# Kernel tuning notes

Hardware: AMD Instinct MI355X
Metric: run time of the kernel (lower is better)

Reference implementation:

```python
import jax, jax.numpy as jnp
import numpy as np

B, D = 1024, 768


def setup_inputs() -> dict:
    key = jax.random.key(0)
    k1, k2 = jax.random.split(key)
    image_features = jax.random.normal(k1, (B, D), dtype=jnp.float32)
    # plant a few exact duplicate rows so the label-propagation path is nontrivial
    image_features = image_features.at[17].set(image_features[3])
    image_features = image_features.at[512].set(image_features[3])
    image_features = image_features.at[900].set(image_features[128])
    text_features = jax.random.normal(k2, (B, D), dtype=jnp.float32)
    logit_scale = jnp.float32(14.285714)  # exp(log(1/0.07)), standard CLIP init
    return {"image_features": image_features, "text_features": text_features, "logit_scale": logit_scale}


def reference(image_features, text_features, logit_scale):
    # logits_per_image: [B, B]
    logits = logit_scale * (image_features @ text_features.T)
    # Duplicate detection: the original O(B^2) python loop assigns to row j the
    # index of the FIRST row i (i <= j) whose features exactly equal row j.
    # eq[i, j] = rows i and j are elementwise identical
    eq = jnp.all(image_features[:, None, :] == image_features[None, :, :], axis=-1)  # [B, B] bool
    labels = jnp.argmax(eq, axis=0)  # first matching index per row (diag guarantees a hit)
    # cross-entropy with integer labels, mean over batch
    logp = jax.nn.log_softmax(logits, axis=1)
    loss = -jnp.mean(jnp.take_along_axis(logp, labels[:, None], axis=1))
    return loss
```

## Files before the change

kernel.cpp:

```cpp
#include <hip/hip_runtime.h>
#include <stdint.h>

#define BATCH 1024
#define DIM 768

typedef unsigned long long u64;
typedef __attribute__((ext_vector_type(8))) short short8;
typedef __attribute__((ext_vector_type(4))) float f32x4;

#define WS_ACC  8192
#define WS_PMAX 12288
#define WS_PSUM 28672
#define WS_TXTB 49152

__device__ __forceinline__ unsigned short to_bf16(float x) {
    unsigned int u = __float_as_uint(x);
    return (unsigned short)((u + 0x7FFFu + ((u >> 16) & 1u)) >> 16);
}

__global__ __launch_bounds__(256) void prep_kernel(
        const float* __restrict__ img, const float* __restrict__ txt,
        u64* __restrict__ hashes, float* __restrict__ acc, int* __restrict__ counter,
        unsigned short* __restrict__ txtB) {
    if (blockIdx.x == 0 && threadIdx.x == 0) { *acc = 0.0f; *counter = 0; }
    const int wave = threadIdx.x >> 6;
    const int lane = threadIdx.x & 63;

    for (int i = wave; i < 6; i += 4) {
        const int G  = blockIdx.x * 6 + i;
        const int tt = G / 24;
        const int g  = G - tt * 24;
        const int col = tt * 16 + (lane & 15);
        const int k0  = g * 32 + (lane >> 4) * 8;
        const float4 va = *(const float4*)(txt + (size_t)col * DIM + k0);
        const float4 vb = *(const float4*)(txt + (size_t)col * DIM + k0 + 4);
        short8 hv = {(short)to_bf16(va.x), (short)to_bf16(va.y),
                     (short)to_bf16(va.z), (short)to_bf16(va.w),
                     (short)to_bf16(vb.x), (short)to_bf16(vb.y),
                     (short)to_bf16(vb.z), (short)to_bf16(vb.w)};
        *(short8*)(txtB + (size_t)(g * 64 + tt) * 512 + lane * 8) = hv;
    }

    const int row = blockIdx.x * 4 + wave;
    const float4* rp = (const float4*)(img + (size_t)row * DIM);
    u64 h = 0;
#pragma unroll
    for (int c = 0; c < 3; ++c) {
        float4 v = rp[c * 64 + lane];
        int p = c * 256 + lane * 4;
        h += ((u64)__float_as_uint(v.x) + 0x9E3779B97F4A7C15ULL) * (u64)(2 * p + 1);
        h += ((u64)__float_as_uint(v.y) + 0x9E3779B97F4A7C15ULL) * (u64)(2 * p + 3);
        h += ((u64)__float_as_uint(v.z) + 0x9E3779B97F4A7C15ULL) * (u64)(2 * p + 5);
        h += ((u64)__float_as_uint(v.w) + 0x9E3779B97F4A7C15ULL) * (u64)(2 * p + 7);
    }
#pragma unroll
    for (int m = 32; m; m >>= 1) h += __shfl_xor(h, m, 64);
    if (lane == 0) hashes[row] = h;
}

__global__ __launch_bounds__(1024) void gemm_kernel(
        const float* __restrict__ img, const float* __restrict__ scale_p,
        const unsigned short* __restrict__ txtB,
        float* __restrict__ pmax, float* __restrict__ psum) {
    __shared__ unsigned short Ahi[16 * DIM];
    __shared__ float logitsS[16 * 260];

    const int tid  = threadIdx.x;
    const int wave = tid >> 6;
    const int lane = tid & 63;
    const int quad = lane >> 4;
    const int l15  = lane & 15;
    const int r0    = (blockIdx.x >> 2) * 16;
    const int chunk = blockIdx.x & 3;

    {
        const float* ir = img + (size_t)(r0 + wave) * DIM;
#pragma unroll
        for (int j = 0; j < 12; ++j) {
            const int k = lane + j * 64;
            Ahi[((k >> 3) * 16 + wave) * 8 + (k & 7)] = to_bf16(ir[k]);
        }
    }
    __syncthreads();

    const int t = chunk * 16 + wave;
    const int foff = quad * 128 + l15 * 8;
    f32x4 acc = {0.f, 0.f, 0.f, 0.f};
#pragma unroll
    for (int kk = 0; kk < 24; ++kk) {
        const short8 a = *(const short8*)&Ahi[kk * 512 + foff];
        const short8 b = *(const short8*)(txtB + (size_t)(kk * 64 + t) * 512 + foff);
        acc = __builtin_amdgcn_mfma_f32_16x16x32_bf16(a, b, acc, 0, 0, 0);
    }

    const float scale = scale_p[0];
#pragma unroll
    for (int r = 0; r < 4; ++r)
        logitsS[(quad * 4 + r) * 260 + wave * 16 + l15] = scale * acc[r];
    __syncthreads();

    {
        const float4 f = *(const float4*)&logitsS[wave * 260 + lane * 4];
        float mx = fmaxf(fmaxf(f.x, f.y), fmaxf(f.z, f.w));
#pragma unroll
        for (int s = 32; s; s >>= 1) mx = fmaxf(mx, __shfl_xor(mx, s, 64));
        float sum = __expf(f.x - mx) + __expf(f.y - mx) +
                    __expf(f.z - mx) + __expf(f.w - mx);
#pragma unroll
        for (int s = 32; s; s >>= 1) sum += __shfl_xor(sum, s, 64);
        if (lane == 0) {
            pmax[(r0 + wave) * 4 + chunk] = mx;
            psum[(r0 + wave) * 4 + chunk] = sum;
        }
    }
}

__global__ __launch_bounds__(1024) void final_kernel(
        const float* __restrict__ img, const float* __restrict__ txt,
        const float* __restrict__ scale_p, const u64* __restrict__ hashes,
        const float* __restrict__ pmax, const float* __restrict__ psum,
        float* __restrict__ acc, int* __restrict__ counter,
        float* __restrict__ out) {
    const int tid  = threadIdx.x;
    const int wave = tid >> 6;
    const int lane = tid & 63;
    const int j = blockIdx.x * 16 + wave;

    const u64 hj = hashes[j];
    int cand = BATCH;
    for (int i = lane; i < j; i += 64)
        if (hashes[i] == hj) { cand = i; break; }
    int label = j;
    for (;;) {
        int mm = cand;
#pragma unroll
        for (int s = 32; s; s >>= 1) mm = min(mm, __shfl_xor(mm, s, 64));
        if (mm >= j) break;
        const float4* rpm = (const float4*)(img + (size_t)mm * DIM);
        const float4* rpj = (const float4*)(img + (size_t)j * DIM);
        bool eq = true;
#pragma unroll
        for (int c = 0; c < 3; ++c) {
            float4 vm = rpm[c * 64 + lane];
            float4 vj = rpj[c * 64 + lane];
            eq = eq && (vm.x == vj.x) && (vm.y == vj.y) &&
                 (vm.z == vj.z) && (vm.w == vj.w);
        }
        if (__all(eq)) { label = mm; break; }
        if (cand == mm) {
            cand = BATCH;
            for (int i = mm + 64; i < j; i += 64)
                if (hashes[i] == hj) { cand = i; break; }
        }
    }

    const float4* aj = (const float4*)(img + (size_t)j * DIM);
    const float4* bl = (const float4*)(txt + (size_t)label * DIM);
    float s = 0.0f;
#pragma unroll
    for (int c = 0; c < 3; ++c) {
        const float4 va = aj[c * 64 + lane];
        const float4 vb = bl[c * 64 + lane];
        s += va.x * vb.x + va.y * vb.y + va.z * vb.z + va.w * vb.w;
    }
#pragma unroll
    for (int m = 32; m; m >>= 1) s += __shfl_xor(s, m, 64);

    if (lane == 0) {
        const float lval = scale_p[0] * s;
        const float m0 = pmax[j * 4 + 0], m1 = pmax[j * 4 + 1];
        const float m2 = pmax[j * 4 + 2], m3 = pmax[j * 4 + 3];
        const float gmax = fmaxf(fmaxf(m0, m1), fmaxf(m2, m3));
        const float ss = psum[j * 4 + 0] * __expf(m0 - gmax)
                       + psum[j * 4 + 1] * __expf(m1 - gmax)
                       + psum[j * 4 + 2] * __expf(m2 - gmax)
                       + psum[j * 4 + 3] * __expf(m3 - gmax);
        const float lse = gmax + __logf(ss);
        atomicAdd(acc, lse - lval);
    }
    __syncthreads();

    if (tid == 0) {
        __threadfence();
        const int old = atomicAdd(counter, 1);
        if (old == (int)gridDim.x - 1) {
            __threadfence();
            out[0] = (*(volatile float*)acc) * (1.0f / BATCH);
        }
    }
}

extern "C" void kernel_launch(void* const* d_in, const int* in_sizes, int n_in,
                              void* d_out, int out_size, void* d_ws, size_t ws_size,
                              hipStream_t stream) {
    const float* img   = (const float*)d_in[0];
    const float* txt   = (const float*)d_in[1];
    const float* scale = (const float*)d_in[2];
    float* out = (float*)d_out;
    char* ws = (char*)d_ws;

    u64*   hashes  = (u64*)ws;
    float* acc     = (float*)(ws + WS_ACC);
    int*   counter = (int*)(ws + WS_ACC + 4);
    float* pmax    = (float*)(ws + WS_PMAX);
    float* psum    = (float*)(ws + WS_PSUM);
    unsigned short* txtB = (unsigned short*)(ws + WS_TXTB);

    prep_kernel<<<256, 256, 0, stream>>>(img, txt, hashes, acc, counter, txtB);
    gemm_kernel<<<256, 1024, 0, stream>>>(img, scale, txtB, pmax, psum);
    final_kernel<<<64, 1024, 0, stream>>>(img, txt, scale, hashes, pmax, psum,
                                          acc, counter, out);
}
```

Measured before the change: 86.33 us.

## Fuse label search and final reduction into GEMM kernel via last-block pattern

Removes the separate final kernel. Each GEMM block's first four waves now do the duplicate-label search and target-logit dot product for four rows, and the last block to finish, detected with an atomic counter, does the log-sum-exp and a deterministic tree reduction of the loss. This saves one kernel launch and the float atomicAdd accumulation, and spreads label work across 256 blocks. In exchange, each wave scans the full hash array with 16 loads, and partial results must be made visible through atomicExch plus threadfence.

Measured after the change: 79.38 us. 1.09x faster.

```diff
diff --git a/kernel.cpp b/kernel.cpp
--- a/kernel.cpp
+++ b/kernel.cpp
@@ -8,9 +8,10 @@
 typedef __attribute__((ext_vector_type(8))) short short8;
 typedef __attribute__((ext_vector_type(4))) float f32x4;
 
-#define WS_ACC  8192
+#define WS_CNT   8192
 #define WS_PMAX 12288
 #define WS_PSUM 28672
+#define WS_LVAL 45056
 #define WS_TXTB 49152
 
 __device__ __forceinline__ unsigned short to_bf16(float x) {
@@ -20,9 +21,9 @@
 
 __global__ __launch_bounds__(256) void prep_kernel(
         const float* __restrict__ img, const float* __restrict__ txt,
-        u64* __restrict__ hashes, float* __restrict__ acc, int* __restrict__ counter,
+        u64* __restrict__ hashes, int* __restrict__ counter,
         unsigned short* __restrict__ txtB) {
-    if (blockIdx.x == 0 && threadIdx.x == 0) { *acc = 0.0f; *counter = 0; }
+    if (blockIdx.x == 0 && threadIdx.x == 0) { *counter = 0; }
     const int wave = threadIdx.x >> 6;
     const int lane = threadIdx.x & 63;
 
@@ -58,12 +59,17 @@
     if (lane == 0) hashes[row] = h;
 }
 
-__global__ __launch_bounds__(1024) void gemm_kernel(
-        const float* __restrict__ img, const float* __restrict__ scale_p,
-        const unsigned short* __restrict__ txtB,
-        float* __restrict__ pmax, float* __restrict__ psum) {
+__global__ __launch_bounds__(1024) void gemm_fused(
+        const float* __restrict__ img, const float* __restrict__ txt,
+        const float* __restrict__ scale_p, const unsigned short* __restrict__ txtB,
+        const u64* __restrict__ hashes,
+        float* __restrict__ pmax, float* __restrict__ psum,
+        float* __restrict__ lval, int* __restrict__ counter,
+        float* __restrict__ out) {
     __shared__ unsigned short Ahi[16 * DIM];
     __shared__ float logitsS[16 * 260];
+    __shared__ int isLast;
+    __shared__ float part[16];
 
     const int tid  = threadIdx.x;
     const int wave = tid >> 6;
@@ -109,83 +115,81 @@
 #pragma unroll
         for (int s = 32; s; s >>= 1) sum += __shfl_xor(sum, s, 64);
         if (lane == 0) {
-            pmax[(r0 + wave) * 4 + chunk] = mx;
-            psum[(r0 + wave) * 4 + chunk] = sum;
-        }
-    }
-}
-
-__global__ __launch_bounds__(1024) void final_kernel(
-        const float* __restrict__ img, const float* __restrict__ txt,
-        const float* __restrict__ scale_p, const u64* __restrict__ hashes,
-        const float* __restrict__ pmax, const float* __restrict__ psum,
-        float* __restrict__ acc, int* __restrict__ counter,
-        float* __restrict__ out) {
-    const int tid  = threadIdx.x;
-    const int wave = tid >> 6;
-    const int lane = tid & 63;
-    const int j = blockIdx.x * 16 + wave;
-
-    const u64 hj = hashes[j];
-    int cand = BATCH;
-    for (int i = lane; i < j; i += 64)
-        if (hashes[i] == hj) { cand = i; break; }
-    int label = j;
-    for (;;) {
-        int mm = cand;
-#pragma unroll
-        for (int s = 32; s; s >>= 1) mm = min(mm, __shfl_xor(mm, s, 64));
-        if (mm >= j) break;
-        const float4* rpm = (const float4*)(img + (size_t)mm * DIM);
-        const float4* rpj = (const float4*)(img + (size_t)j * DIM);
-        bool eq = true;
+            atomicExch(&pmax[(r0 + wave) * 4 + chunk], mx);
+            atomicExch(&psum[(r0 + wave) * 4 + chunk], sum);
+        }
+    }
+
+    if (wave < 4) {
+        const int j = r0 + chunk * 4 + wave;
+        const u64 hj = hashes[j];
+        int lo = -1;
+        int label = j;
+        for (;;) {
+            int cand = BATCH;
+#pragma unroll
+            for (int it = 0; it < 16; ++it) {
+                const int i = lane + it * 64;
+                const u64 h = hashes[i];
+                if (i < j && i > lo && h == hj) cand = min(cand, i);
+            }
+#pragma unroll
+            for (int s = 32; s; s >>= 1) cand = min(cand, __shfl_xor(cand, s, 64));
+            if (cand >= j) break;
+            const float4* rpm = (const float4*)(img + (size_t)cand * DIM);
+            const float4* rpj = (const float4*)(img + (size_t)j * DIM);
+            bool eq = true;
+#pragma unroll
+            for (int c = 0; c < 3; ++c) {
+                float4 vm = rpm[c * 64 + lane];
+                float4 vj = rpj[c * 64 + lane];
+                eq = eq && (vm.x == vj.x) && (vm.y == vj.y) &&
+                     (vm.z == vj.z) && (vm.w == vj.w);
+            }
+            if (__all(eq)) { label = cand; break; }
+            lo = cand;
+        }
+
+        const float4* aj = (const float4*)(img + (size_t)j * DIM);
+        const float4* bl = (const float4*)(txt + (size_t)label * DIM);
+        float s = 0.0f;
 #pragma unroll
         for (int c = 0; c < 3; ++c) {
-            float4 vm = rpm[c * 64 + lane];
-            float4 vj = rpj[c * 64 + lane];
-            eq = eq && (vm.x == vj.x) && (vm.y == vj.y) &&
-                 (vm.z == vj.z) && (vm.w == vj.w);
-        }
-        if (__all(eq)) { label = mm; break; }
-        if (cand == mm) {
-            cand = BATCH;
-            for (int i = mm + 64; i < j; i += 64)
-                if (hashes[i] == hj) { cand = i; break; }
-        }
-    }
-
-    const float4* aj = (const float4*)(img + (size_t)j * DIM);
-    const float4* bl = (const float4*)(txt + (size_t)label * DIM);
-    float s = 0.0f;
-#pragma unroll
-    for (int c = 0; c < 3; ++c) {
-        const float4 va = aj[c * 64 + lane];
-        const float4 vb = bl[c * 64 + lane];
-        s += va.x * vb.x + va.y * vb.y + va.z * vb.z + va.w * vb.w;
-    }
-#pragma unroll
-    for (int m = 32; m; m >>= 1) s += __shfl_xor(s, m, 64);
-
-    if (lane == 0) {
-        const float lval = scale_p[0] * s;
-        const float m0 = pmax[j * 4 + 0], m1 = pmax[j * 4 + 1];
-        const float m2 = pmax[j * 4 + 2], m3 = pmax[j * 4 + 3];
-        const float gmax = fmaxf(fmaxf(m0, m1), fmaxf(m2, m3));
-        const float ss = psum[j * 4 + 0] * __expf(m0 - gmax)
-                       + psum[j * 4 + 1] * __expf(m1 - gmax)
-                       + psum[j * 4 + 2] * __expf(m2 - gmax)
-                       + psum[j * 4 + 3] * __expf(m3 - gmax);
-        const float lse = gmax + __logf(ss);
-        atomicAdd(acc, lse - lval);
-    }
-    __syncthreads();
-
+            const float4 va = aj[c * 64 + lane];
+            const float4 vb = bl[c * 64 + lane];
+            s += va.x * vb.x + va.y * vb.y + va.z * vb.z + va.w * vb.w;
+        }
+#pragma unroll
+        for (int m = 32; m; m >>= 1) s += __shfl_xor(s, m, 64);
+        if (lane == 0) atomicExch(&lval[j], scale * s);
+    }
+
+    __syncthreads();
     if (tid == 0) {
         __threadfence();
-        const int old = atomicAdd(counter, 1);
-        if (old == (int)gridDim.x - 1) {
-            __threadfence();
-            out[0] = (*(volatile float*)acc) * (1.0f / BATCH);
+        isLast = (atomicAdd(counter, 1) == (int)gridDim.x - 1) ? 1 : 0;
+    }
+    __syncthreads();
+    if (!isLast) return;
+    __threadfence();
+
+    {
+        const float4 m4 = *(const float4*)&pmax[tid * 4];
+        const float4 s4 = *(const float4*)&psum[tid * 4];
+        const float lv = lval[tid];
+        const float gmax = fmaxf(fmaxf(m4.x, m4.y), fmaxf(m4.z, m4.w));
+        const float ss = s4.x * __expf(m4.x - gmax) + s4.y * __expf(m4.y - gmax)
+                       + s4.z * __expf(m4.z - gmax) + s4.w * __expf(m4.w - gmax);
+        float loss = gmax + __logf(ss) - lv;
+#pragma unroll
+        for (int m = 32; m; m >>= 1) loss += __shfl_xor(loss, m, 64);
+        if (lane == 0) part[wave] = loss;
+        __syncthreads();
+        if (tid == 0) {
+            float tot = 0.0f;
+#pragma unroll
+            for (int w = 0; w < 16; ++w) tot += part[w];
+            out[0] = tot * (1.0f / BATCH);
         }
     }
 }
@@ -200,14 +204,13 @@
     char* ws = (char*)d_ws;
 
     u64*   hashes  = (u64*)ws;
-    float* acc     = (float*)(ws + WS_ACC);
-    int*   counter = (int*)(ws + WS_ACC + 4);
+    int*   counter = (int*)(ws + WS_CNT);
     float* pmax    = (float*)(ws + WS_PMAX);
     float* psum    = (float*)(ws + WS_PSUM);
+    float* lval    = (float*)(ws + WS_LVAL);
     unsigned short* txtB = (unsigned short*)(ws + WS_TXTB);
 
-    prep_kernel<<<256, 256, 0, stream>>>(img, txt, hashes, acc, counter, txtB);
-    gemm_kernel<<<256, 1024, 0, stream>>>(img, scale, txtB, pmax, psum);
-    final_kernel<<<64, 1024, 0, stream>>>(img, txt, scale, hashes, pmax, psum,
-                                          acc, counter, out);
-}
+    prep_kernel<<<256, 256, 0, stream>>>(img, txt, hashes, counter, txtB);
+    gemm_fused<<<256, 1024, 0, stream>>>(img, txt, scale, txtB, hashes,
+                                         pmax, psum, lval, counter, out);
+}
```
